# Kernel tuning notes

Measured on AMD Instinct MI355X. Metric: run time of the kernel, lower is better.

## Reference

```python
import jax, jax.numpy as jnp
import numpy as np

NUM_USER = 100000
NUM_ITEM = 50000
N_NODES = NUM_USER + NUM_ITEM
DIM_E = 64
N_EDGES = 2_000_000  # user-item interactions; symmetric adj nnz = 2*N_EDGES
N_LAYERS = 3
DROP_RATE = 0.5
BATCH = 16384


def setup_inputs() -> dict:
    key = jax.random.key(0)
    k_u, k_i, k_ue, k_ie, k_m, k_bu, k_bi = jax.random.split(key, 7)
    # bipartite interaction edges -> symmetric adjacency (COO)
    u = jax.random.randint(k_u, (N_EDGES,), 0, NUM_USER, dtype=jnp.int32)
    it = jax.random.randint(k_i, (N_EDGES,), 0, NUM_ITEM, dtype=jnp.int32) + NUM_USER
    adj_row = jnp.concatenate([u, it])          # [4M]
    adj_col = jnp.concatenate([it, u])          # [4M]
    # symmetric normalization D^-1/2 A D^-1/2
    deg = jnp.zeros((N_NODES,), jnp.float32).at[adj_row].add(1.0) + 1e-7
    dinv = deg ** -0.5
    adj_val = dinv[adj_row] * dinv[adj_col]     # [4M]
    # xavier-uniform-ish embeddings
    ue_scale = (6.0 / (NUM_USER + DIM_E)) ** 0.5
    ie_scale = (6.0 / (NUM_ITEM + DIM_E)) ** 0.5
    user_emb = jax.random.uniform(k_ue, (NUM_USER, DIM_E), jnp.float32, -ue_scale, ue_scale)
    item_emb = jax.random.uniform(k_ie, (NUM_ITEM, DIM_E), jnp.float32, -ie_scale, ie_scale)
    # fixed sparse-dropout keep mask (rate=0.5)
    drop_mask = jax.random.uniform(k_m, (2 * N_EDGES,)) < (1.0 - DROP_RATE)
    users = jax.random.randint(k_bu, (BATCH,), 0, NUM_USER, dtype=jnp.int64)
    items = jax.random.randint(k_bi, (BATCH,), 0, NUM_ITEM, dtype=jnp.int64)
    return {"user_emb": user_emb, "item_emb": item_emb, "adj_val": adj_val,
            "adj_row": adj_row, "adj_col": adj_col, "drop_mask": drop_mask,
            "users": users, "items": items}


def reference(user_emb, item_emb, adj_val, adj_row, adj_col, drop_mask, users, items):
    # sparse dropout: drop entries, rescale kept ones by 1/(1-rate)
    val = jnp.where(drop_mask, adj_val * (1.0 / (1.0 - DROP_RATE)), 0.0)
    ego = jnp.concatenate([user_emb, item_emb], axis=0)   # [N, D]
    acc = ego
    for _ in range(N_LAYERS):
        # SpMM: out[r] += val * ego[c]
        ego = jax.ops.segment_sum(val[:, None] * ego[adj_col], adj_row,
                                  num_segments=N_NODES)
        acc = acc + ego
    all_emb = acc / (N_LAYERS + 1)                        # mean over stacked layers
    user_embeddings = all_emb[users]
    item_embeddings = all_emb[NUM_USER + items]
    return (user_embeddings, item_embeddings)
```

## Files before the change

### kernel.cpp

```cpp
#include <hip/hip_runtime.h>
#include <hip/hip_bf16.h>


#define NUSER 100000
#define NITEM 50000
#define NNODE 150000
#define DIM   64
#define NNZ   4000000
#define BATCH 16384

#define BSH2  9
#define BRWS  512
#define NBK   293
#define SCAP  2048
#define BCAP  16384
#define CHUNK 4096
#define GP1   977
#define GCC   4688
#define GGF   1024
#define GSP   4688
#define GOUT  2048

typedef __hip_bfloat16 bf16;
typedef unsigned short ushort;
typedef unsigned long long u64;
typedef float f4 __attribute__((ext_vector_type(4)));
typedef ushort us4 __attribute__((ext_vector_type(4)));
typedef ushort us8 __attribute__((ext_vector_type(8)));

__device__ __forceinline__ float loadF(const void* p, long i, int isbf16) {
    return isbf16 ? __bfloat162float(((const bf16*)p)[i]) : ((const float*)p)[i];
}

__device__ __forceinline__ bool keepE(const void* mask, int e, int isbyte) {
    return isbyte ? (((const unsigned char*)mask)[e] != 0)
                  : (((const int*)mask)[e] != 0);
}

__device__ __forceinline__ ushort f2bf(float x) {
    unsigned u = __float_as_uint(x);
    return (ushort)((u + 0x7FFFu + ((u >> 16) & 1u)) >> 16);
}
__device__ __forceinline__ float bf2f(ushort u) {
    return __uint_as_float((unsigned)u << 16);
}

__device__ __forceinline__ unsigned encodeV(float v) {
    unsigned fb = __float_as_uint(v);
    unsigned e8 = (fb >> 23) & 0xFFu;
    unsigned m7 = (fb >> 16) & 0x7Fu;
    return ((e8 - 95u) << 7) | m7;
}
__device__ __forceinline__ float decodeV(unsigned code) {
    unsigned vb = code >> 18;
    return __uint_as_float((((vb >> 7) + 95u) << 23) | ((vb & 0x7Fu) << 16));
}

__device__ __forceinline__ long nodeOf(int b, const int* users, const int* items, int sh) {
    if (b < BATCH) return (long)users[(size_t)b << sh];
    return (long)NUSER + (long)items[(size_t)(b - BATCH) << sh];
}

__global__ __launch_bounds__(256) void detect_fmt(const unsigned int* __restrict__ mask,
                                                  const unsigned int* __restrict__ users,
                                                  const unsigned int* __restrict__ adjv,
                                                  int* __restrict__ flags,
                                                  int* __restrict__ bcur) {
    __shared__ int s[3];
    if (threadIdx.x < 3) s[threadIdx.x] = 0;
    for (int b = threadIdx.x; b < 8 * NBK; b += 256) bcur[b] = 0;
    __syncthreads();
    int c0 = 0, c1 = 0, c2 = 0;
    for (int i = threadIdx.x; i < 4096; i += 256) {
        c0 += (mask[i] > 1u) ? 1 : 0;
        if (i & 1) c1 += (users[i] == 0u) ? 1 : 0;
        unsigned lo = adjv[i] & 0xFFFFu;
        unsigned ex = (lo >> 7) & 0xFFu;
        c2 += ((lo >> 15) == 0u && ex >= 0x60u && ex <= 0x7Fu) ? 1 : 0;
    }
    atomicAdd(&s[0], c0); atomicAdd(&s[1], c1); atomicAdd(&s[2], c2);
    __syncthreads();
    if (threadIdx.x == 0) {
        flags[0] = (s[0] > 16) ? 1 : 0;
        flags[1] = (s[1] > 1024) ? 1 : 0;
        flags[2] = (s[2] > 3000) ? 1 : 0;
    }
}

__global__ __launch_bounds__(512) void prep_fused(const void* __restrict__ mask,
                                                  const int* __restrict__ rows,
                                                  const int* __restrict__ cols,
                                                  const void* __restrict__ adjv,
                                                  const void* __restrict__ ue,
                                                  const void* __restrict__ ie,
                                                  const int* __restrict__ users,
                                                  const int* __restrict__ items,
                                                  const int* __restrict__ flags,
                                                  int* __restrict__ bcur,
                                                  u64* __restrict__ part,
                                                  ushort* __restrict__ A,
                                                  float* __restrict__ out_acc) {
    __shared__ int cnt[NBK];
    __shared__ int cur[NBK];
    const int blk = blockIdx.x;
    const int tid = threadIdx.x;

    if (blk < GP1) {
        const int isbyte = flags[0];
        const int isbf = flags[2];
        const int base_e = blk * CHUNK;
        const int sh = blk & 7;
        u64 rec[8];
        int bkt[8], off[8];
        unsigned kept = 0;

        for (int b = tid; b < NBK; b += 512) cnt[b] = 0;
        __syncthreads();

        #pragma unroll
        for (int k = 0; k < 8; ++k) {
            int e = base_e + k * 512 + tid;
            if (e < NNZ && keepE(mask, e, isbyte)) {
                int r = rows[e];
                float v = 2.0f * loadF(adjv, e, isbf);
                rec[k] = (u64)(unsigned)(r & (BRWS - 1))
                       | ((u64)(unsigned)cols[e] << 9)
                       | ((u64)encodeV(v) << 27);
                bkt[k] = r >> BSH2;
                off[k] = atomicAdd(&cnt[bkt[k]], 1);
                kept |= 1u << k;
            }
        }
        __syncthreads();

        for (int b = tid; b < NBK; b += 512)
            cur[b] = cnt[b] ? atomicAdd(&bcur[sh * NBK + b], cnt[b]) : 0;
        __syncthreads();

        #pragma unroll
        for (int k = 0; k < 8; ++k) {
            if (kept & (1u << k)) {
                int pos = cur[bkt[k]] + off[k];
                if (pos < SCAP)
                    part[(size_t)bkt[k] * BCAP + sh * SCAP + pos] = rec[k];
            }
        }
    } else if (blk < GP1 + GCC) {
        long q = (long)(blk - GP1) * 512 + tid;
        const long NU4 = (long)NUSER * DIM / 4;
        const long NT4 = (long)NNODE * DIM / 4;
        if (q >= NT4) return;
        us4 o;
        if (!flags[2]) {
            const f4* s = (q < NU4) ? (const f4*)ue : (const f4*)ie;
            f4 v = s[(q < NU4) ? q : q - NU4];
            o[0] = f2bf(v.x); o[1] = f2bf(v.y); o[2] = f2bf(v.z); o[3] = f2bf(v.w);
        } else {
            const us4* s = (q < NU4) ? (const us4*)ue : (const us4*)ie;
            o = s[(q < NU4) ? q : q - NU4];
        }
        ((us4*)A)[q] = o;
    } else {
        int t = (blk - GP1 - GCC) * 512 + tid;
        if (t >= 2 * BATCH * DIM / 4) return;
        long node = nodeOf(t >> 4, users, items, flags[1]);
        int d4 = t & 15;
        const void* src = (node < NUSER) ? ue : ie;
        long q = (node < NUSER ? node : node - NUSER) * 16 + d4;
        f4 a;
        if (!flags[2]) {
            a = ((const f4*)src)[q];
        } else {
            us4 u = ((const us4*)src)[q];
            a.x = bf2f(u[0]); a.y = bf2f(u[1]); a.z = bf2f(u[2]); a.w = bf2f(u[3]);
        }
        ((f4*)out_acc)[t] = a;
    }
}

__global__ __launch_bounds__(512) void pass2_csr(const u64* __restrict__ part,
                                                 const int* __restrict__ bcur,
                                                 unsigned* __restrict__ edges,
                                                 int* __restrict__ rowptr) {
    __shared__ int tot[512];
    __shared__ int cnt[BRWS];
    __shared__ int ex[BRWS];
    __shared__ int wsum[512];
    __shared__ int ns[8];
    __shared__ int gb_s;
    int b = blockIdx.x;
    int tid = threadIdx.x;

    int v = 0;
    if (tid < NBK) {
        #pragma unroll
        for (int sh = 0; sh < 8; ++sh) {
            int c = bcur[sh * NBK + tid];
            v += (c > SCAP) ? SCAP : c;
        }
    }
    tot[tid] = v;
    if (tid < 8) {
        int c = bcur[tid * NBK + b];
        ns[tid] = (c > SCAP) ? SCAP : c;
    }
    cnt[tid] = 0;
    __syncthreads();
    for (int off = 1; off < 512; off <<= 1) {
        int t = (tid >= off) ? tot[tid - off] : 0;
        __syncthreads();
        tot[tid] += t;
        __syncthreads();
    }
    if (tid == 0) {
        gb_s = (b > 0) ? tot[b - 1] : 0;
        if (b == 0) rowptr[0] = 0;
    }
    __syncthreads();
    const int gb = gb_s;
    const u64* bp = part + (size_t)b * BCAP;

    #pragma unroll
    for (int sh = 0; sh < 8; ++sh) {
        int n = ns[sh];
        const u64* rp = bp + sh * SCAP;
        for (int j = tid; j < n; j += 512)
            atomicAdd(&cnt[(int)(rp[j] & (BRWS - 1))], 1);
    }
    __syncthreads();

    int c = cnt[tid];
    wsum[tid] = c;
    __syncthreads();
    for (int off = 1; off < 512; off <<= 1) {
        int t = (tid >= off) ? wsum[tid - off] : 0;
        __syncthreads();
        wsum[tid] += t;
        __syncthreads();
    }
    int incl = wsum[tid];
    ex[tid] = incl - c;
    int gr = (b << BSH2) + tid;
    if (gr < NNODE) rowptr[gr + 1] = gb + incl;
    __syncthreads();

    #pragma unroll
    for (int sh = 0; sh < 8; ++sh) {
        int n = ns[sh];
        const u64* rp = bp + sh * SCAP;
        for (int j = tid; j < n; j += 512) {
            u64 rec = rp[j];
            int r = (int)(rec & (BRWS - 1));
            int pos = atomicAdd(&ex[r], 1);
            unsigned col = (unsigned)((rec >> 9) & 0x3FFFFu);
            unsigned code = (unsigned)((rec >> 27) & 0x1FFFu);
            edges[gb + pos] = col | (code << 18);
        }
    }
}

__global__ __launch_bounds__(256) void spmm_fused(const ushort* __restrict__ src,
                                                  const int* __restrict__ rowptr,
                                                  const unsigned* __restrict__ edges,
                                                  ushort* __restrict__ dst,
                                                  const int* __restrict__ users,
                                                  const int* __restrict__ items,
                                                  const int* __restrict__ flags,
                                                  float* __restrict__ acc) {
    if (blockIdx.x >= GSP) {
        int t = (blockIdx.x - GSP) * 256 + threadIdx.x;
        if (t >= 2 * BATCH * DIM / 4) return;
        long node = nodeOf(t >> 4, users, items, flags[1]);
        us4 u = ((const us4*)(src + node * DIM))[t & 15];
        f4 a = ((f4*)acc)[t];
        a.x += bf2f(u[0]); a.y += bf2f(u[1]); a.z += bf2f(u[2]); a.w += bf2f(u[3]);
        ((f4*)acc)[t] = a;
        return;
    }
    int r = blockIdx.x * 32 + (threadIdx.x >> 3);
    if (r >= NNODE) return;
    int t = threadIdx.x & 7;
    int j0 = rowptr[r], j1 = rowptr[r + 1];
    float acc8[8] = {0, 0, 0, 0, 0, 0, 0, 0};
    int j = j0;
    for (; j + 4 <= j1; j += 4) {
        unsigned e0 = edges[j];
        unsigned e1 = edges[j + 1];
        unsigned e2 = edges[j + 2];
        unsigned e3 = edges[j + 3];
        us8 s0 = ((const us8*)(src + (size_t)(e0 & 0x3FFFFu) * DIM))[t];
        us8 s1 = ((const us8*)(src + (size_t)(e1 & 0x3FFFFu) * DIM))[t];
        us8 s2 = ((const us8*)(src + (size_t)(e2 & 0x3FFFFu) * DIM))[t];
        us8 s3 = ((const us8*)(src + (size_t)(e3 & 0x3FFFFu) * DIM))[t];
        float v0 = decodeV(e0), v1 = decodeV(e1);
        float v2 = decodeV(e2), v3 = decodeV(e3);
        #pragma unroll
        for (int d = 0; d < 8; ++d) {
            acc8[d] += v0 * bf2f(s0[d]);
            acc8[d] += v1 * bf2f(s1[d]);
            acc8[d] += v2 * bf2f(s2[d]);
            acc8[d] += v3 * bf2f(s3[d]);
        }
    }
    for (; j < j1; ++j) {
        unsigned e0 = edges[j];
        float v0 = decodeV(e0);
        us8 s0 = ((const us8*)(src + (size_t)(e0 & 0x3FFFFu) * DIM))[t];
        #pragma unroll
        for (int d = 0; d < 8; ++d) acc8[d] += v0 * bf2f(s0[d]);
    }
    us8 o;
    #pragma unroll
    for (int d = 0; d < 8; ++d) o[d] = f2bf(acc8[d]);
    __builtin_nontemporal_store(o, (us8*)(dst + (size_t)r * DIM) + t);
}

__global__ __launch_bounds__(256) void gather_final(const ushort* __restrict__ table,
                                                    const int* __restrict__ users,
                                                    const int* __restrict__ items,
                                                    const int* __restrict__ flags,
                                                    const float* __restrict__ acc,
                                                    float* __restrict__ out) {
    int t = blockIdx.x * 256 + threadIdx.x;
    if (t >= 2 * BATCH * DIM / 4) return;
    long node = nodeOf(t >> 4, users, items, flags[1]);
    us4 u = ((const us4*)(table + node * DIM))[t & 15];
    f4 a = ((const f4*)acc)[t];
    a.x = 0.25f * (a.x + bf2f(u[0]));
    a.y = 0.25f * (a.y + bf2f(u[1]));
    a.z = 0.25f * (a.z + bf2f(u[2]));
    a.w = 0.25f * (a.w + bf2f(u[3]));
    __builtin_nontemporal_store(a, (f4*)out + t);
}

extern "C" void kernel_launch(void* const* d_in, const int* in_sizes, int n_in,
                              void* d_out, int out_size, void* d_ws, size_t ws_size,
                              hipStream_t stream) {
    const void* user_emb = d_in[0];
    const void* item_emb = d_in[1];
    const void* adj_val  = d_in[2];
    const int*  adj_row  = (const int*)d_in[3];
    const int*  adj_col  = (const int*)d_in[4];
    const void* drop_msk = d_in[5];
    const int*  users    = (const int*)d_in[6];
    const int*  items    = (const int*)d_in[7];
    float* out = (float*)d_out;

    char* ws = (char*)d_ws;
    size_t off = 0;
    int* flags = (int*)(ws + off);            off += 256;
    float* out_acc = (float*)(ws + off);      off += (size_t)2 * BATCH * DIM * 4;
    ushort* A = (ushort*)(ws + off);          off += (size_t)NNODE * DIM * 2;
    ushort* B = (ushort*)(ws + off);          off += (size_t)NNODE * DIM * 2;
    int* rowptr = (int*)(ws + off);           off += 600064;
    int* bcur = (int*)(ws + off);             off += 16384;
    u64* part = (u64*)(ws + off);             off += (size_t)NBK * BCAP * 8;
    unsigned* edges = (unsigned*)(ws + off);  off += (size_t)NNZ * 4;

    detect_fmt<<<1, 256, 0, stream>>>((const unsigned int*)drop_msk,
                                      (const unsigned int*)users,
                                      (const unsigned int*)adj_val, flags, bcur);
    prep_fused<<<GP1 + GCC + GGF, 512, 0, stream>>>(drop_msk, adj_row, adj_col,
                                                    adj_val, user_emb, item_emb,
                                                    users, items, flags, bcur,
                                                    part, A, out_acc);
    pass2_csr<<<NBK, 512, 0, stream>>>(part, bcur, edges, rowptr);

    spmm_fused<<<GSP, 256, 0, stream>>>(A, rowptr, edges, B,
                                        users, items, flags, out_acc);
    spmm_fused<<<GSP + GOUT, 256, 0, stream>>>(B, rowptr, edges, A,
                                               users, items, flags, out_acc);
    spmm_fused<<<GSP + GOUT, 256, 0, stream>>>(A, rowptr, edges, B,
                                               users, items, flags, out_acc);
    gather_final<<<GOUT, 256, 0, stream>>>(B, users, items, flags, out_acc, out);
}
```

Before: 188.7 us.

## Compute the last propagation layer only for batch rows and fuse with gather

The third SpMM layer used to be computed over all 150k nodes and then gathered. It is replaced by a kernel that computes the layer-3 row only for the 32k requested users and items, then adds the layer-2 embedding and the running accumulator before writing the mean. This drops most of the last SpMM's edge traffic and one launch. The risk is load imbalance, since each row is handled by one 8-thread group.

```diff
diff --git a/kernel.cpp b/kernel.cpp
--- a/kernel.cpp
+++ b/kernel.cpp
@@ -20,6 +20,7 @@
 #define GGF   1024
 #define GSP   4688
 #define GOUT  2048
+#define GFIN  1024
 
 typedef __hip_bfloat16 bf16;
 typedef unsigned short ushort;
@@ -315,22 +316,62 @@
     __builtin_nontemporal_store(o, (us8*)(dst + (size_t)r * DIM) + t);
 }
 
-__global__ __launch_bounds__(256) void gather_final(const ushort* __restrict__ table,
-                                                    const int* __restrict__ users,
-                                                    const int* __restrict__ items,
-                                                    const int* __restrict__ flags,
-                                                    const float* __restrict__ acc,
-                                                    float* __restrict__ out) {
-    int t = blockIdx.x * 256 + threadIdx.x;
-    if (t >= 2 * BATCH * DIM / 4) return;
-    long node = nodeOf(t >> 4, users, items, flags[1]);
-    us4 u = ((const us4*)(table + node * DIM))[t & 15];
-    f4 a = ((const f4*)acc)[t];
-    a.x = 0.25f * (a.x + bf2f(u[0]));
-    a.y = 0.25f * (a.y + bf2f(u[1]));
-    a.z = 0.25f * (a.z + bf2f(u[2]));
-    a.w = 0.25f * (a.w + bf2f(u[3]));
-    __builtin_nontemporal_store(a, (f4*)out + t);
+__global__ __launch_bounds__(256) void final_fused(const ushort* __restrict__ A,
+                                                   const int* __restrict__ rowptr,
+                                                   const unsigned* __restrict__ edges,
+                                                   const int* __restrict__ users,
+                                                   const int* __restrict__ items,
+                                                   const int* __restrict__ flags,
+                                                   const float* __restrict__ acc,
+                                                   float* __restrict__ out) {
+    int b = blockIdx.x * 32 + (threadIdx.x >> 3);
+    if (b >= 2 * BATCH) return;
+    int t = threadIdx.x & 7;
+    long node = nodeOf(b, users, items, flags[1]);
+    int j0 = rowptr[node], j1 = rowptr[node + 1];
+    float a8[8] = {0, 0, 0, 0, 0, 0, 0, 0};
+    int j = j0;
+    for (; j + 4 <= j1; j += 4) {
+        unsigned e0 = edges[j];
+        unsigned e1 = edges[j + 1];
+        unsigned e2 = edges[j + 2];
+        unsigned e3 = edges[j + 3];
+        us8 s0 = ((const us8*)(A + (size_t)(e0 & 0x3FFFFu) * DIM))[t];
+        us8 s1 = ((const us8*)(A + (size_t)(e1 & 0x3FFFFu) * DIM))[t];
+        us8 s2 = ((const us8*)(A + (size_t)(e2 & 0x3FFFFu) * DIM))[t];
+        us8 s3 = ((const us8*)(A + (size_t)(e3 & 0x3FFFFu) * DIM))[t];
+        float v0 = decodeV(e0), v1 = decodeV(e1);
+        float v2 = decodeV(e2), v3 = decodeV(e3);
+        #pragma unroll
+        for (int d = 0; d < 8; ++d) {
+            a8[d] += v0 * bf2f(s0[d]);
+            a8[d] += v1 * bf2f(s1[d]);
+            a8[d] += v2 * bf2f(s2[d]);
+            a8[d] += v3 * bf2f(s3[d]);
+        }
+    }
+    for (; j < j1; ++j) {
+        unsigned e0 = edges[j];
+        float v0 = decodeV(e0);
+        us8 s0 = ((const us8*)(A + (size_t)(e0 & 0x3FFFFu) * DIM))[t];
+        #pragma unroll
+        for (int d = 0; d < 8; ++d) a8[d] += v0 * bf2f(s0[d]);
+    }
+    us8 u2 = ((const us8*)(A + node * DIM))[t];
+    const f4* ap = (const f4*)acc + (size_t)b * 16 + 2 * t;
+    f4 a0 = ap[0], a1 = ap[1];
+    f4 o0, o1;
+    o0.x = 0.25f * (a0.x + bf2f(u2[0]) + a8[0]);
+    o0.y = 0.25f * (a0.y + bf2f(u2[1]) + a8[1]);
+    o0.z = 0.25f * (a0.z + bf2f(u2[2]) + a8[2]);
+    o0.w = 0.25f * (a0.w + bf2f(u2[3]) + a8[3]);
+    o1.x = 0.25f * (a1.x + bf2f(u2[4]) + a8[4]);
+    o1.y = 0.25f * (a1.y + bf2f(u2[5]) + a8[5]);
+    o1.z = 0.25f * (a1.z + bf2f(u2[6]) + a8[6]);
+    o1.w = 0.25f * (a1.w + bf2f(u2[7]) + a8[7]);
+    f4* op = (f4*)(out + (size_t)b * DIM) + 2 * t;
+    __builtin_nontemporal_store(o0, op);
+    __builtin_nontemporal_store(o1, op + 1);
 }
 
 extern "C" void kernel_launch(void* const* d_in, const int* in_sizes, int n_in,
@@ -370,7 +411,6 @@
                                         users, items, flags, out_acc);
     spmm_fused<<<GSP + GOUT, 256, 0, stream>>>(B, rowptr, edges, A,
                                                users, items, flags, out_acc);
-    spmm_fused<<<GSP + GOUT, 256, 0, stream>>>(A, rowptr, edges, B,
-                                               users, items, flags, out_acc);
-    gather_final<<<GOUT, 256, 0, stream>>>(B, users, items, flags, out_acc, out);
-}
+    final_fused<<<GFIN, 256, 0, stream>>>(A, rowptr, edges, users, items,
+                                          flags, out_acc, out);
+}
```

After: 163.8 us. -13.2%, faster.
